# Optimization experiments

Hardware: AMD Instinct MI355X
Metric: run time of the kernel (lower is better)

## Reference

```python
import jax, jax.numpy as jnp
import numpy as np
import math

N, H, E, G = 20000, 256, 320000, 1000
NF, NS = 64, 3           # sinusoid frequencies, spatial dims
DIS = 2 * NF * NS        # 384
EIN = 2 * H + 9 + DIS    # edge MLP input dim = 905


def silu(x):
    return x * jax.nn.sigmoid(x)


def sin_emb(x):
    # x: [E, 3] -> [E, 2*NF*3]
    freqs = 2.0 * math.pi * jnp.arange(NF, dtype=x.dtype)
    emb = (x[..., None] * freqs).reshape(x.shape[0], NF * NS)
    return jnp.concatenate([jnp.sin(emb), jnp.cos(emb)], axis=-1)


def layer_norm(x, gamma, beta, eps=1e-5):
    mu = jnp.mean(x, axis=-1, keepdims=True)
    var = jnp.var(x, axis=-1, keepdims=True)
    return (x - mu) * jax.lax.rsqrt(var + eps) * gamma + beta


def setup_inputs() -> dict:
    key = jax.random.key(0)
    ks = jax.random.split(key, 16)
    s = 0.02
    return {
        "node_features": jax.random.normal(ks[0], (N, H), jnp.float32),
        "lattices": jax.random.normal(ks[1], (G, 3, 3), jnp.float32),
        "edge_index": jax.random.randint(ks[2], (2, E), 0, N, dtype=jnp.int64),
        "edge2graph": jnp.sort(jax.random.randint(ks[3], (E,), 0, G, dtype=jnp.int64)),
        "frac_diff": jax.random.uniform(ks[4], (E, NS), jnp.float32),
        "num_atoms": jax.random.randint(ks[5], (G,), 0, 100, dtype=jnp.int64),
        "ln_gamma": jnp.ones((H,), jnp.float32),
        "ln_beta": jnp.zeros((H,), jnp.float32),
        "We1": jax.random.normal(ks[6], (EIN, H), jnp.float32) * s,
        "be1": jnp.zeros((H,), jnp.float32),
        "We2": jax.random.normal(ks[7], (H, H), jnp.float32) * s,
        "be2": jnp.zeros((H,), jnp.float32),
        "Wn1": jax.random.normal(ks[8], (2 * H, H), jnp.float32) * s,
        "bn1": jnp.zeros((H,), jnp.float32),
        "Wn2": jax.random.normal(ks[9], (H, H), jnp.float32) * s,
        "bn2": jnp.zeros((H,), jnp.float32),
    }


def reference(node_features, lattices, edge_index, edge2graph, frac_diff, num_atoms,
              ln_gamma, ln_beta, We1, be1, We2, be2, Wn1, bn1, Wn2, bn2):
    n = node_features.shape[0]
    h = layer_norm(node_features, ln_gamma, ln_beta)

    # edge model: gather + concat + MLP
    hi = h[edge_index[0]]                      # [E, H]
    hj = h[edge_index[1]]                      # [E, H]
    fd = sin_emb(frac_diff)                    # [E, DIS]
    ltl = jnp.einsum('gij,gkj->gik', lattices, lattices).reshape(-1, 9)  # non_symmetric: L @ L^T
    le = ltl[edge2graph]                       # [E, 9]
    x = jnp.concatenate([hi, hj, le, fd], axis=1)        # [E, EIN]
    e = silu(x @ We1 + be1)
    e = silu(e @ We2 + be2)                    # [E, H]

    # node model: scatter-mean + concat + MLP
    src = edge_index[0]
    sums = jax.ops.segment_sum(e, src, num_segments=n)   # [N, H]
    cnt = jax.ops.segment_sum(jnp.ones((e.shape[0],), e.dtype), src, num_segments=n)
    agg = sums / jnp.maximum(cnt, 1.0)[:, None]
    y = jnp.concatenate([h, agg], axis=1)                # [N, 2H]
    y = silu(y @ Wn1 + bn1)
    y = silu(y @ Wn2 + bn2)

    return node_features + y
```

## Files before the change

kernel.cpp:

```cpp
#include <hip/hip_runtime.h>

typedef unsigned short UST;
typedef __bf16 bf16x8 __attribute__((ext_vector_type(8)));
typedef float floatx4 __attribute__((ext_vector_type(4)));
typedef unsigned short ushort8v __attribute__((ext_vector_type(8)));
typedef unsigned short ushort4v __attribute__((ext_vector_type(4)));

#define N_NODES 20000
#define E_EDGES 320000
#define KE 928
#define M_PAD 20096

static __device__ __forceinline__ UST f2bf(float x){
  unsigned int u = __float_as_uint(x);
  u += 0x7fffu + ((u >> 16) & 1u);
  return (UST)(u >> 16);
}
static __device__ __forceinline__ float bf2f(UST u){
  return __uint_as_float(((unsigned int)u) << 16);
}
static __device__ __forceinline__ float siluf(float v){
  return v / (1.0f + __expf(-v));
}
static __device__ __forceinline__ void gll16(const void* g, void* lds){
  __builtin_amdgcn_global_load_lds(
      (const __attribute__((address_space(1))) unsigned int*)g,
      (__attribute__((address_space(3))) unsigned int*)lds, 16, 0, 0);
}

static __device__ __forceinline__ void mfma_step(const UST* As, const UST* Bs,
    floatx4 (&acc)[4][4], int lm, int quad, int wM, int wN){
  bf16x8 a[4], b[4];
#pragma unroll
  for (int i = 0; i < 4; ++i)
    a[i] = *(const bf16x8*)(As + (wM + i*16 + lm)*32 + quad*8);
#pragma unroll
  for (int i = 0; i < 4; ++i)
    b[i] = *(const bf16x8*)(Bs + (wN + i*16 + lm)*32 + quad*8);
#pragma unroll
  for (int mi = 0; mi < 4; ++mi)
#pragma unroll
    for (int ni = 0; ni < 4; ++ni)
      acc[mi][ni] = __builtin_amdgcn_mfma_f32_16x16x32_bf16(a[mi], b[ni], acc[mi][ni], 0, 0, 0);
}

static __device__ __forceinline__ void mfma_stage2(const UST* At, const UST* Bg,
    int Kb, floatx4 (&acc)[4][4], int lm, int quad, int wM, int wN){
#pragma unroll 2
  for (int k0 = 0; k0 < 256; k0 += 32){
    bf16x8 a[4], b[4];
#pragma unroll
    for (int i = 0; i < 4; ++i)
      a[i] = *(const bf16x8*)(At + (wM + i*16 + lm)*264 + k0 + quad*8);
#pragma unroll
    for (int i = 0; i < 4; ++i)
      b[i] = *(const bf16x8*)(Bg + (size_t)(wN + i*16 + lm)*Kb + k0 + quad*8);
#pragma unroll
    for (int mi = 0; mi < 4; ++mi)
#pragma unroll
      for (int ni = 0; ni < 4; ++ni)
        acc[mi][ni] = __builtin_amdgcn_mfma_f32_16x16x32_bf16(a[mi], b[ni], acc[mi][ni], 0, 0, 0);
  }
}

__global__ __launch_bounds__(256) void prep_all(
    const float* __restrict__ We1, const float* __restrict__ We2,
    const float* __restrict__ Wn1, const float* __restrict__ Wn2,
    const float* __restrict__ x, const float* __restrict__ gamma,
    const float* __restrict__ beta, const float* __restrict__ lat,
    const int* __restrict__ esrc, int* __restrict__ cnti,
    UST* __restrict__ W1T, UST* __restrict__ W2T,
    UST* __restrict__ Wn1T, UST* __restrict__ Wn2T,
    UST* __restrict__ h, float* __restrict__ ltl){
  int bid = blockIdx.x, t = threadIdx.x;
  if (bid < 928){
    int i = bid*256 + t;
    int n = i / KE, k = i % KE;
    float v = 0.0f;
    if (k < 512)      v = We1[(size_t)k*256 + n];
    else if (k < 896){
      int idx = k - 512, j = idx >> 1, b = idx & 1;
      v = We1[(size_t)(521 + b*192 + j)*256 + n];
    }
    else if (k < 905) v = We1[(size_t)(k-384)*256 + n];
    W1T[i] = f2bf(v);
  } else if (bid < 1184){
    int i = (bid-928)*256 + t;
    int n = i >> 8, k = i & 255;
    W2T[i]  = f2bf(We2[(size_t)k*256 + n]);
    Wn2T[i] = f2bf(Wn2[(size_t)k*256 + n]);
  } else if (bid < 1696){
    int i = (bid-1184)*256 + t;
    int n = i >> 9, k = i & 511;
    Wn1T[i] = f2bf(Wn1[(size_t)k*256 + n]);
  } else if (bid < 6696){
    int wave = t >> 6, lane = t & 63;
    int row = (bid-1696)*4 + wave;
    const float4* xp = (const float4*)(x + (size_t)row * 256);
    float4 v = xp[lane];
    float s  = v.x + v.y + v.z + v.w;
    float sq = v.x*v.x + v.y*v.y + v.z*v.z + v.w*v.w;
#pragma unroll
    for (int o = 32; o > 0; o >>= 1){ s += __shfl_xor(s, o); sq += __shfl_xor(sq, o); }
    float mu  = s * (1.0f/256.0f);
    float var = sq * (1.0f/256.0f) - mu*mu;
    float rs  = rsqrtf(var + 1e-5f);
    float4 g = ((const float4*)gamma)[lane];
    float4 b = ((const float4*)beta)[lane];
    ushort4v o4;
    o4[0] = f2bf((v.x-mu)*rs*g.x + b.x);
    o4[1] = f2bf((v.y-mu)*rs*g.y + b.y);
    o4[2] = f2bf((v.z-mu)*rs*g.z + b.z);
    o4[3] = f2bf((v.w-mu)*rs*g.w + b.w);
    *(ushort4v*)(h + (size_t)row*256 + lane*4) = o4;
  } else if (bid < 6732){
    int i = (bid-6696)*256 + t;
    if (i < 9000){
      int g = i / 9, ij = i % 9, a = ij / 3, b = ij % 3;
      const float* L = lat + g*9;
      ltl[i] = L[a*3+0]*L[b*3+0] + L[a*3+1]*L[b*3+1] + L[a*3+2]*L[b*3+2];
    }
  } else {
    int e = (bid-6732)*256 + t;
    if (e < E_EDGES) atomicAdd(&cnti[esrc[e]], 1);
  }
}

__global__ __launch_bounds__(256) void scan_kernel(const int* __restrict__ cnti,
    int* __restrict__ off, int* __restrict__ head){
  __shared__ int ps[256];
  int t = threadIdx.x;
  const int CH = 80;
  const int4* cp = (const int4*)cnti;
  int base = t * CH;
  int s = 0;
#pragma unroll 1
  for (int i = 0; i < CH/4; ++i){
    int4 v = cp[t*(CH/4) + i];
    int idx = base + i*4;
    if (idx   < N_NODES) s += v.x;
    if (idx+1 < N_NODES) s += v.y;
    if (idx+2 < N_NODES) s += v.z;
    if (idx+3 < N_NODES) s += v.w;
  }
  ps[t] = s; __syncthreads();
#pragma unroll 1
  for (int o = 1; o < 256; o <<= 1){
    int v = (t >= o) ? ps[t - o] : 0;
    __syncthreads();
    ps[t] += v;
    __syncthreads();
  }
  int run = (t > 0) ? ps[t-1] : 0;
#pragma unroll 1
  for (int i = 0; i < CH/4; ++i){
    int4 v = cp[t*(CH/4) + i];
    int idx = base + i*4;
    int a4[4] = {v.x, v.y, v.z, v.w};
#pragma unroll
    for (int j = 0; j < 4; ++j){
      int id = idx + j;
      if (id < N_NODES){ off[id] = run; head[id] = run; run += a4[j]; }
    }
  }
  if (t == 255) off[N_NODES] = run;
}

__global__ __launch_bounds__(256) void fill_kernel(const int* __restrict__ src,
    int* __restrict__ head, int* __restrict__ eidx, int* __restrict__ srcs){
  int e = blockIdx.x*256 + threadIdx.x;
  if (e < E_EDGES){
    int s = src[e];
    int p = atomicAdd(&head[s], 1);
    eidx[p] = e;
    srcs[p] = s;
  }
}

__global__ __launch_bounds__(512, 4)
void gemm_edge_fused(const UST* __restrict__ h, const int* __restrict__ ei,
                     const int* __restrict__ e2g, const float* __restrict__ fdif,
                     const float* __restrict__ ltl, const UST* __restrict__ W1T,
                     const float* __restrict__ be1, const int* __restrict__ eidx,
                     const UST* __restrict__ W2T, const float* __restrict__ be2,
                     const int* __restrict__ rownode, float* __restrict__ sums){
  __shared__ __attribute__((aligned(16))) UST lds[128*264];
  __shared__ int rn[128];
  UST* As0 = lds;
  UST* As1 = lds + 4096;
  UST* Bs0 = lds + 8192;
  UST* Bs1 = lds + 16384;
  UST* e1t = lds;
  UST* EsT = lds;
  int t = threadIdx.x;
  int bM = blockIdx.x;
  int rA = t >> 2, cA = (t & 3) * 8;
  int p0 = bM*128 + rA;
  int e0 = eidx[p0];
  int src0 = ei[e0];
  int dst0 = ei[E_EDGES + e0];
  int g0 = e2g[e0];
  float f0x = fdif[e0*3+0], f0y = fdif[e0*3+1], f0z = fdif[e0*3+2];
  size_t btb0 = (size_t)rA*KE + cA;
  size_t btb1 = btb0 + (size_t)128*KE;
  int lane = t & 63, lm = lane & 15, quad = lane >> 4;
  int wave = t >> 6, wM = (wave >> 2)*64, wN = (wave & 3)*64;
  floatx4 acc[4][4] = {};
  UST* a0d = &As0[rA*32 + cA];
  UST* a1d = &As1[rA*32 + cA];
  UST* b0d0 = &Bs0[rA*32 + cA];
  UST* b0d1 = &Bs0[(128+rA)*32 + cA];
  UST* b1d0 = &Bs1[rA*32 + cA];
  UST* b1d1 = &Bs1[(128+rA)*32 + cA];
  if (t < 128) rn[t] = rownode[bM*128 + t];

#pragma unroll 1
  for (int w = 0; w < 8; ++w){
    int k0 = w*64;
    const UST* srow = (w < 4) ? (h + (size_t)src0*256 + k0)
                              : (h + (size_t)dst0*256 + (k0 - 256));
    gll16(srow + cA,      a0d);
    gll16(srow + 32 + cA, a1d);
    gll16(W1T + btb0 + k0,      b0d0);
    gll16(W1T + btb1 + k0,      b0d1);
    gll16(W1T + btb0 + k0 + 32, b1d0);
    gll16(W1T + btb1 + k0 + 32, b1d1);
    __syncthreads();
    mfma_step(As0, Bs0, acc, lm, quad, wM, wN);
    mfma_step(As1, Bs1, acc, lm, quad, wM, wN);
    __syncthreads();
  }
#pragma unroll 1
  for (int w = 8; w < 14; ++w){
    int k0 = w*64;
    gll16(W1T + btb0 + k0,      b0d0);
    gll16(W1T + btb1 + k0,      b0d1);
    gll16(W1T + btb0 + k0 + 32, b1d0);
    gll16(W1T + btb1 + k0 + 32, b1d1);
    int jb0 = (k0 + cA - 512) >> 1;
    ushort8v o0, o1;
#pragma unroll
    for (int ii = 0; ii < 4; ++ii){
      int jj = jb0 + ii;
      int dim = jj >> 6; float kf = (float)(jj & 63);
      float fr = (dim == 0) ? f0x : ((dim == 1) ? f0y : f0z);
      float q = __builtin_amdgcn_fractf(fr * kf);
      o0[2*ii]   = f2bf(__builtin_amdgcn_sinf(q));
      o0[2*ii+1] = f2bf(__builtin_amdgcn_cosf(q));
    }
#pragma unroll
    for (int ii = 0; ii < 4; ++ii){
      int jj = jb0 + 16 + ii;
      int dim = jj >> 6; float kf = (float)(jj & 63);
      float fr = (dim == 0) ? f0x : ((dim == 1) ? f0y : f0z);
      float q = __builtin_amdgcn_fractf(fr * kf);
      o1[2*ii]   = f2bf(__builtin_amdgcn_sinf(q));
      o1[2*ii+1] = f2bf(__builtin_amdgcn_cosf(q));
    }
    *(ushort8v*)a0d = o0;
    *(ushort8v*)a1d = o1;
    __syncthreads();
    mfma_step(As0, Bs0, acc, lm, quad, wM, wN);
    mfma_step(As1, Bs1, acc, lm, quad, wM, wN);
    __syncthreads();
  }
  {
    gll16(W1T + btb0 + 896, b0d0);
    gll16(W1T + btb1 + 896, b0d1);
    ushort8v o0;
#pragma unroll
    for (int i = 0; i < 8; ++i){
      int c = cA + i;
      o0[i] = (c < 9) ? f2bf(ltl[g0*9 + c]) : (UST)0;
    }
    *(ushort8v*)a0d = o0;
    __syncthreads();
    mfma_step(As0, Bs0, acc, lm, quad, wM, wN);
  }
  __syncthreads();
#pragma unroll
  for (int mi = 0; mi < 4; ++mi)
#pragma unroll
    for (int r = 0; r < 4; ++r){
      int ml = wM + mi*16 + quad*4 + r;
#pragma unroll
      for (int ni = 0; ni < 4; ++ni){
        int nl = wN + ni*16 + lm;
        float v = acc[mi][ni][r] + be1[nl];
        e1t[ml*264 + nl] = f2bf(siluf(v));
      }
    }
  __syncthreads();

  floatx4 acc2[4][4] = {};
  mfma_stage2(e1t, W2T, 256, acc2, lm, quad, wM, wN);
  __syncthreads();

#pragma unroll
  for (int mi = 0; mi < 4; ++mi)
#pragma unroll
    for (int ni = 0; ni < 4; ++ni){
      int nl = wN + ni*16 + lm;
      int ml = wM + mi*16 + quad*4;
      ushort4v pk;
#pragma unroll
      for (int r = 0; r < 4; ++r)
        pk[r] = f2bf(siluf(acc2[mi][ni][r] + be2[nl]));
      *(ushort4v*)&EsT[nl*132 + ml] = pk;
    }
  __syncthreads();
  {
    int c = t & 255, hh = t >> 8;
    int rbeg = hh * 64;
    int cur = rn[rbeg];
    float run = 0.0f;
#pragma unroll 1
    for (int r = rbeg; r < rbeg + 64; r += 4){
      ushort4v v4 = *(const ushort4v*)&EsT[c*132 + r];
#pragma unroll
      for (int q2 = 0; q2 < 4; ++q2){
        int nd = rn[r + q2];
        if (nd != cur){ atomicAdd(&sums[(size_t)cur*256 + c], run); run = 0.0f; cur = nd; }
        run += bf2f(v4[q2]);
      }
    }
    atomicAdd(&sums[(size_t)cur*256 + c], run);
  }
}

__global__ __launch_bounds__(512, 4)
void gemm_node12(const UST* __restrict__ h, const float* __restrict__ sums,
                 const int* __restrict__ offs, const UST* __restrict__ B1,
                 const float* __restrict__ bn1, const UST* __restrict__ B2,
                 const float* __restrict__ bn2,
                 float* __restrict__ out_f, const float* __restrict__ resid){
  __shared__ __attribute__((aligned(16))) UST lds[128*264];
  UST* As0 = lds;
  UST* As1 = lds + 4096;
  UST* Bs0 = lds + 8192;
  UST* Bs1 = lds + 16384;
  UST* y1t = lds;
  int t = threadIdx.x;
  int bM = blockIdx.x;
  int rA = t >> 2, cA = (t & 3) * 8;
  int row = bM*128 + rA;
  bool valid = row < N_NODES;
  float inv = 0.0f;
  if (valid){
    int deg = offs[row+1] - offs[row];
    inv = 1.0f / fmaxf((float)deg, 1.0f);
  }
  const UST* hrow = h + (size_t)row*256;
  const float* srow = sums + (size_t)row*256;
  size_t bb0 = (size_t)rA*512 + cA;
  size_t bb1 = bb0 + (size_t)128*512;
  int lane = t & 63, lm = lane & 15, quad = lane >> 4;
  int wave = t >> 6, wM = (wave >> 2)*64, wN = (wave & 3)*64;
  floatx4 acc[4][4] = {};
  UST* a0d = &As0[rA*32 + cA];
  UST* a1d = &As1[rA*32 + cA];
  UST* b0d0 = &Bs0[rA*32 + cA];
  UST* b0d1 = &Bs0[(128+rA)*32 + cA];
  UST* b1d0 = &Bs1[rA*32 + cA];
  UST* b1d1 = &Bs1[(128+rA)*32 + cA];
  const ushort8v z8 = {0,0,0,0,0,0,0,0};
#pragma unroll 1
  for (int w = 0; w < 8; ++w){
    int k0 = w*64;
    if (k0 < 256){
      if (valid){
        gll16(hrow + k0 + cA,      a0d);
        gll16(hrow + k0 + 32 + cA, a1d);
      } else {
        *(ushort8v*)a0d = z8;
        *(ushort8v*)a1d = z8;
      }
    } else {
      ushort8v o0 = z8, o1 = z8;
      if (valid){
        int q = k0 - 256 + cA;
        float4 s0 = *(const float4*)(srow + q);
        float4 s1 = *(const float4*)(srow + q + 4);
        o0[0]=f2bf(s0.x*inv); o0[1]=f2bf(s0.y*inv); o0[2]=f2bf(s0.z*inv); o0[3]=f2bf(s0.w*inv);
        o0[4]=f2bf(s1.x*inv); o0[5]=f2bf(s1.y*inv); o0[6]=f2bf(s1.z*inv); o0[7]=f2bf(s1.w*inv);
        float4 s2 = *(const float4*)(srow + q + 32);
        float4 s3 = *(const float4*)(srow + q + 36);
        o1[0]=f2bf(s2.x*inv); o1[1]=f2bf(s2.y*inv); o1[2]=f2bf(s2.z*inv); o1[3]=f2bf(s2.w*inv);
        o1[4]=f2bf(s3.x*inv); o1[5]=f2bf(s3.y*inv); o1[6]=f2bf(s3.z*inv); o1[7]=f2bf(s3.w*inv);
      }
      *(ushort8v*)a0d = o0;
      *(ushort8v*)a1d = o1;
    }
    gll16(B1 + bb0 + k0,      b0d0);
    gll16(B1 + bb1 + k0,      b0d1);
    gll16(B1 + bb0 + k0 + 32, b1d0);
    gll16(B1 + bb1 + k0 + 32, b1d1);
    __syncthreads();
    mfma_step(As0, Bs0, acc, lm, quad, wM, wN);
    mfma_step(As1, Bs1, acc, lm, quad, wM, wN);
    __syncthreads();
  }
  __syncthreads();
#pragma unroll
  for (int mi = 0; mi < 4; ++mi)
#pragma unroll
    for (int r = 0; r < 4; ++r){
      int ml = wM + mi*16 + quad*4 + r;
#pragma unroll
      for (int ni = 0; ni < 4; ++ni){
        int nl = wN + ni*16 + lm;
        y1t[ml*264 + nl] = f2bf(siluf(acc[mi][ni][r] + bn1[nl]));
      }
    }
  __syncthreads();
  floatx4 acc2[4][4] = {};
  mfma_stage2(y1t, B2, 256, acc2, lm, quad, wM, wN);
  int mbase = bM*128 + wM + quad*4;
  int nbase = wN + lm;
#pragma unroll
  for (int mi = 0; mi < 4; ++mi)
#pragma unroll
    for (int r = 0; r < 4; ++r){
      int m = mbase + mi*16 + r;
      if (m < N_NODES){
#pragma unroll
        for (int ni = 0; ni < 4; ++ni){
          int n = nbase + ni*16;
          float v = siluf(acc2[mi][ni][r] + bn2[n]);
          out_f[(size_t)m*256 + n] = resid[(size_t)m*256 + n] + v;
        }
      }
    }
}

extern "C" void kernel_launch(void* const* d_in, const int* in_sizes, int n_in,
                              void* d_out, int out_size, void* d_ws, size_t ws_size,
                              hipStream_t stream){
  (void)in_sizes; (void)n_in; (void)out_size; (void)ws_size;
  const float* node_features = (const float*)d_in[0];
  const float* lattices      = (const float*)d_in[1];
  const int*   edge_index    = (const int*)d_in[2];
  const int*   edge2graph    = (const int*)d_in[3];
  const float* frac_diff     = (const float*)d_in[4];
  const float* ln_gamma      = (const float*)d_in[6];
  const float* ln_beta       = (const float*)d_in[7];
  const float* We1 = (const float*)d_in[8];
  const float* be1 = (const float*)d_in[9];
  const float* We2 = (const float*)d_in[10];
  const float* be2 = (const float*)d_in[11];
  const float* Wn1 = (const float*)d_in[12];
  const float* bn1 = (const float*)d_in[13];
  const float* Wn2 = (const float*)d_in[14];
  const float* bn2 = (const float*)d_in[15];

  char* w = (char*)d_ws;
  size_t off_b = 0;
  auto carve = [&](size_t bytes) -> char* {
    char* p = w + off_b; off_b += (bytes + 1023) & ~(size_t)1023; return p;
  };
  UST*   W1T  = (UST*)carve((size_t)256*KE*2);
  UST*   W2T  = (UST*)carve((size_t)256*256*2);
  UST*   Wn1T = (UST*)carve((size_t)256*512*2);
  UST*   Wn2T = (UST*)carve((size_t)256*256*2);
  UST*   hbf  = (UST*)carve((size_t)N_NODES*256*2);
  float* ltl  = (float*)carve((size_t)9000*4);
  int*   cnti = (int*)carve((size_t)20480*4);
  int*   offs = (int*)carve((size_t)(N_NODES+1)*4);
  int*   head = (int*)carve((size_t)N_NODES*4);
  int*   eidx = (int*)carve((size_t)E_EDGES*4);
  int*   srcs = (int*)carve((size_t)E_EDGES*4);
  float* sums = (float*)carve((size_t)N_NODES*256*4);

  hipMemsetAsync(cnti, 0, (size_t)20480*4, stream);
  hipMemsetAsync(sums, 0, (size_t)N_NODES*256*4, stream);

  prep_all<<<6732 + E_EDGES/256, 256, 0, stream>>>(We1, We2, Wn1, Wn2,
      node_features, ln_gamma, ln_beta, lattices, edge_index, cnti,
      W1T, W2T, Wn1T, Wn2T, hbf, ltl);

  scan_kernel<<<1, 256, 0, stream>>>(cnti, offs, head);
  fill_kernel<<<E_EDGES/256, 256, 0, stream>>>(edge_index, head, eidx, srcs);

  gemm_edge_fused<<<E_EDGES/128, 512, 0, stream>>>(
      hbf, edge_index, edge2graph, frac_diff, ltl, W1T, be1, eidx,
      W2T, be2, srcs, sums);

  gemm_node12<<<M_PAD/128, 512, 0, stream>>>(
      hbf, sums, offs, Wn1T, bn1, Wn2T, bn2, (float*)d_out, node_features);
}
```

Before: 493.6 us.

## Precompute per-node and per-graph edge-MLP projections to shrink edge GEMM K

Splits the first edge-MLP layer by linearity. The h_src and h_dst parts are computed once per node in a new node-level GEMM (P1 = h @ We1[:512], with N=512 outputs). The lattice and bias parts are folded into a per-graph vector (Pleb). The edge GEMM now only contracts over the 384 sinusoid features and gathers fp32 P1/Pleb rows in its epilogue. This removes the per-edge gather of h and cuts edge GEMM K from 928 to 384. In exchange it adds a ~41MB fp32 P1 buffer and random fp32 gathers in the epilogue, and the hidden inputs now sum in fp32 rather than bf16.

```diff
diff --git a/kernel.cpp b/kernel.cpp
--- a/kernel.cpp
+++ b/kernel.cpp
@@ -8,7 +8,7 @@
 
 #define N_NODES 20000
 #define E_EDGES 320000
-#define KE 928
+#define KF 384
 #define M_PAD 20096
 
 static __device__ __forceinline__ UST f2bf(float x){
@@ -68,34 +68,31 @@
     const float* __restrict__ Wn1, const float* __restrict__ Wn2,
     const float* __restrict__ x, const float* __restrict__ gamma,
     const float* __restrict__ beta, const float* __restrict__ lat,
-    const int* __restrict__ esrc, int* __restrict__ cnti,
+    const int* __restrict__ esrc, const float* __restrict__ be1,
+    int* __restrict__ cnti,
     UST* __restrict__ W1T, UST* __restrict__ W2T,
-    UST* __restrict__ Wn1T, UST* __restrict__ Wn2T,
-    UST* __restrict__ h, float* __restrict__ ltl){
+    UST* __restrict__ Wn1T, UST* __restrict__ Wn2T, UST* __restrict__ W1hT,
+    UST* __restrict__ h, float* __restrict__ Pleb){
   int bid = blockIdx.x, t = threadIdx.x;
-  if (bid < 928){
+  if (bid < 384){
     int i = bid*256 + t;
-    int n = i / KE, k = i % KE;
-    float v = 0.0f;
-    if (k < 512)      v = We1[(size_t)k*256 + n];
-    else if (k < 896){
-      int idx = k - 512, j = idx >> 1, b = idx & 1;
-      v = We1[(size_t)(521 + b*192 + j)*256 + n];
-    }
-    else if (k < 905) v = We1[(size_t)(k-384)*256 + n];
-    W1T[i] = f2bf(v);
-  } else if (bid < 1184){
-    int i = (bid-928)*256 + t;
+    int n = i / KF, k = i % KF;
+    W1T[i] = f2bf(We1[(size_t)(521 + (k&1)*192 + (k>>1))*256 + n]);
+  } else if (bid < 640){
+    int i = (bid-384)*256 + t;
     int n = i >> 8, k = i & 255;
     W2T[i]  = f2bf(We2[(size_t)k*256 + n]);
     Wn2T[i] = f2bf(Wn2[(size_t)k*256 + n]);
-  } else if (bid < 1696){
-    int i = (bid-1184)*256 + t;
+  } else if (bid < 1152){
+    int i = (bid-640)*256 + t;
     int n = i >> 9, k = i & 511;
     Wn1T[i] = f2bf(Wn1[(size_t)k*256 + n]);
-  } else if (bid < 6696){
+  } else if (bid < 1664){
+    int n = bid - 1152, k = t;
+    W1hT[n*256 + k] = f2bf(We1[(size_t)(k + (n & 256))*256 + (n & 255)]);
+  } else if (bid < 6664){
     int wave = t >> 6, lane = t & 63;
-    int row = (bid-1696)*4 + wave;
+    int row = (bid-1664)*4 + wave;
     const float4* xp = (const float4*)(x + (size_t)row * 256);
     float4 v = xp[lane];
     float s  = v.x + v.y + v.z + v.w;
@@ -113,15 +110,20 @@
     o4[2] = f2bf((v.z-mu)*rs*g.z + b.z);
     o4[3] = f2bf((v.w-mu)*rs*g.w + b.w);
     *(ushort4v*)(h + (size_t)row*256 + lane*4) = o4;
-  } else if (bid < 6732){
-    int i = (bid-6696)*256 + t;
-    if (i < 9000){
-      int g = i / 9, ij = i % 9, a = ij / 3, b = ij % 3;
-      const float* L = lat + g*9;
-      ltl[i] = L[a*3+0]*L[b*3+0] + L[a*3+1]*L[b*3+1] + L[a*3+2]*L[b*3+2];
-    }
+  } else if (bid < 7664){
+    int g = bid - 6664;
+    const float* L = lat + g*9;
+    float acc = be1[t];
+#pragma unroll
+    for (int a = 0; a < 3; ++a)
+#pragma unroll
+      for (int b = 0; b < 3; ++b){
+        float ltlv = L[a*3+0]*L[b*3+0] + L[a*3+1]*L[b*3+1] + L[a*3+2]*L[b*3+2];
+        acc += ltlv * We1[(size_t)(512 + a*3 + b)*256 + t];
+      }
+    Pleb[g*256 + t] = acc;
   } else {
-    int e = (bid-6732)*256 + t;
+    int e = (bid-7664)*256 + t;
     if (e < E_EDGES) atomicAdd(&cnti[esrc[e]], 1);
   }
 }
@@ -178,14 +180,66 @@
 }
 
 __global__ __launch_bounds__(512, 4)
-void gemm_edge_fused(const UST* __restrict__ h, const int* __restrict__ ei,
-                     const int* __restrict__ e2g, const float* __restrict__ fdif,
-                     const float* __restrict__ ltl, const UST* __restrict__ W1T,
-                     const float* __restrict__ be1, const int* __restrict__ eidx,
+void gemm_p1(const UST* __restrict__ h, const UST* __restrict__ B1,
+             float* __restrict__ P1){
+  __shared__ __attribute__((aligned(16))) UST lds[24576];
+  UST* As0 = lds;
+  UST* As1 = lds + 4096;
+  UST* Bs0 = lds + 8192;
+  UST* Bs1 = lds + 16384;
+  int t = threadIdx.x;
+  int bM = blockIdx.x >> 1, bN = (blockIdx.x & 1) << 8;
+  int rA = t >> 2, cA = (t & 3) * 8;
+  const UST* hrow = h + (size_t)(bM*128 + rA)*256;
+  size_t bb0 = (size_t)(bN + rA)*256 + cA;
+  size_t bb1 = bb0 + (size_t)128*256;
+  int lane = t & 63, lm = lane & 15, quad = lane >> 4;
+  int wave = t >> 6, wM = (wave >> 2)*64, wN = (wave & 3)*64;
+  floatx4 acc[4][4] = {};
+  UST* a0d = &As0[rA*32 + cA];
+  UST* a1d = &As1[rA*32 + cA];
+  UST* b0d0 = &Bs0[rA*32 + cA];
+  UST* b0d1 = &Bs0[(128+rA)*32 + cA];
+  UST* b1d0 = &Bs1[rA*32 + cA];
+  UST* b1d1 = &Bs1[(128+rA)*32 + cA];
+#pragma unroll 1
+  for (int w = 0; w < 4; ++w){
+    int k0 = w*64;
+    gll16(hrow + k0 + cA,      a0d);
+    gll16(hrow + k0 + 32 + cA, a1d);
+    gll16(B1 + bb0 + k0,      b0d0);
+    gll16(B1 + bb1 + k0,      b0d1);
+    gll16(B1 + bb0 + k0 + 32, b1d0);
+    gll16(B1 + bb1 + k0 + 32, b1d1);
+    __syncthreads();
+    mfma_step(As0, Bs0, acc, lm, quad, wM, wN);
+    mfma_step(As1, Bs1, acc, lm, quad, wM, wN);
+    __syncthreads();
+  }
+  int mbase = bM*128 + wM + quad*4;
+#pragma unroll
+  for (int mi = 0; mi < 4; ++mi)
+#pragma unroll
+    for (int r = 0; r < 4; ++r){
+      int m = mbase + mi*16 + r;
+#pragma unroll
+      for (int ni = 0; ni < 4; ++ni){
+        int n = bN + wN + ni*16 + lm;
+        P1[(size_t)m*512 + n] = acc[mi][ni][r];
+      }
+    }
+}
+
+__global__ __launch_bounds__(512, 4)
+void gemm_edge_fused(const int* __restrict__ ei, const int* __restrict__ e2g,
+                     const float* __restrict__ fdif, const UST* __restrict__ W1T,
+                     const int* __restrict__ eidx,
                      const UST* __restrict__ W2T, const float* __restrict__ be2,
-                     const int* __restrict__ rownode, float* __restrict__ sums){
+                     const int* __restrict__ rownode,
+                     const float* __restrict__ P1, const float* __restrict__ Pleb,
+                     float* __restrict__ sums){
   __shared__ __attribute__((aligned(16))) UST lds[128*264];
-  __shared__ int rn[128];
+  __shared__ int rn[128], rd[128], rg[128];
   UST* As0 = lds;
   UST* As1 = lds + 4096;
   UST* Bs0 = lds + 8192;
@@ -197,12 +251,9 @@
   int rA = t >> 2, cA = (t & 3) * 8;
   int p0 = bM*128 + rA;
   int e0 = eidx[p0];
-  int src0 = ei[e0];
-  int dst0 = ei[E_EDGES + e0];
-  int g0 = e2g[e0];
   float f0x = fdif[e0*3+0], f0y = fdif[e0*3+1], f0z = fdif[e0*3+2];
-  size_t btb0 = (size_t)rA*KE + cA;
-  size_t btb1 = btb0 + (size_t)128*KE;
+  size_t btb0 = (size_t)rA*KF + cA;
+  size_t btb1 = btb0 + (size_t)128*KF;
   int lane = t & 63, lm = lane & 15, quad = lane >> 4;
   int wave = t >> 6, wM = (wave >> 2)*64, wN = (wave & 3)*64;
   floatx4 acc[4][4] = {};
@@ -212,32 +263,21 @@
   UST* b0d1 = &Bs0[(128+rA)*32 + cA];
   UST* b1d0 = &Bs1[rA*32 + cA];
   UST* b1d1 = &Bs1[(128+rA)*32 + cA];
-  if (t < 128) rn[t] = rownode[bM*128 + t];
-
-#pragma unroll 1
-  for (int w = 0; w < 8; ++w){
-    int k0 = w*64;
-    const UST* srow = (w < 4) ? (h + (size_t)src0*256 + k0)
-                              : (h + (size_t)dst0*256 + (k0 - 256));
-    gll16(srow + cA,      a0d);
-    gll16(srow + 32 + cA, a1d);
-    gll16(W1T + btb0 + k0,      b0d0);
-    gll16(W1T + btb1 + k0,      b0d1);
-    gll16(W1T + btb0 + k0 + 32, b1d0);
-    gll16(W1T + btb1 + k0 + 32, b1d1);
-    __syncthreads();
-    mfma_step(As0, Bs0, acc, lm, quad, wM, wN);
-    mfma_step(As1, Bs1, acc, lm, quad, wM, wN);
-    __syncthreads();
-  }
-#pragma unroll 1
-  for (int w = 8; w < 14; ++w){
+  if (t < 128){
+    int e = eidx[bM*128 + t];
+    rn[t] = rownode[bM*128 + t];
+    rd[t] = ei[E_EDGES + e];
+    rg[t] = e2g[e];
+  }
+
+#pragma unroll 1
+  for (int w = 0; w < 6; ++w){
     int k0 = w*64;
     gll16(W1T + btb0 + k0,      b0d0);
     gll16(W1T + btb1 + k0,      b0d1);
     gll16(W1T + btb0 + k0 + 32, b1d0);
     gll16(W1T + btb1 + k0 + 32, b1d1);
-    int jb0 = (k0 + cA - 512) >> 1;
+    int jb0 = (k0 + cA) >> 1;
     ushort8v o0, o1;
 #pragma unroll
     for (int ii = 0; ii < 4; ++ii){
@@ -264,29 +304,20 @@
     mfma_step(As1, Bs1, acc, lm, quad, wM, wN);
     __syncthreads();
   }
-  {
-    gll16(W1T + btb0 + 896, b0d0);
-    gll16(W1T + btb1 + 896, b0d1);
-    ushort8v o0;
-#pragma unroll
-    for (int i = 0; i < 8; ++i){
-      int c = cA + i;
-      o0[i] = (c < 9) ? f2bf(ltl[g0*9 + c]) : (UST)0;
-    }
-    *(ushort8v*)a0d = o0;
-    __syncthreads();
-    mfma_step(As0, Bs0, acc, lm, quad, wM, wN);
-  }
-  __syncthreads();
+
 #pragma unroll
   for (int mi = 0; mi < 4; ++mi)
 #pragma unroll
     for (int r = 0; r < 4; ++r){
       int ml = wM + mi*16 + quad*4 + r;
+      int s = rn[ml], d = rd[ml], g = rg[ml];
+      const float* ps = P1 + (size_t)s*512;
+      const float* pd = P1 + (size_t)d*512 + 256;
+      const float* pg = Pleb + (size_t)g*256;
 #pragma unroll
       for (int ni = 0; ni < 4; ++ni){
         int nl = wN + ni*16 + lm;
-        float v = acc[mi][ni][r] + be1[nl];
+        float v = acc[mi][ni][r] + ps[nl] + pd[nl] + pg[nl];
         e1t[ml*264 + nl] = f2bf(siluf(v));
       }
     }
@@ -458,12 +489,14 @@
   auto carve = [&](size_t bytes) -> char* {
     char* p = w + off_b; off_b += (bytes + 1023) & ~(size_t)1023; return p;
   };
-  UST*   W1T  = (UST*)carve((size_t)256*KE*2);
+  UST*   W1T  = (UST*)carve((size_t)256*KF*2);
   UST*   W2T  = (UST*)carve((size_t)256*256*2);
   UST*   Wn1T = (UST*)carve((size_t)256*512*2);
   UST*   Wn2T = (UST*)carve((size_t)256*256*2);
-  UST*   hbf  = (UST*)carve((size_t)N_NODES*256*2);
-  float* ltl  = (float*)carve((size_t)9000*4);
+  UST*   W1hT = (UST*)carve((size_t)512*256*2);
+  UST*   hbf  = (UST*)carve((size_t)M_PAD*256*2);
+  float* P1   = (float*)carve((size_t)M_PAD*512*4);
+  float* Pleb = (float*)carve((size_t)1000*256*4);
   int*   cnti = (int*)carve((size_t)20480*4);
   int*   offs = (int*)carve((size_t)(N_NODES+1)*4);
   int*   head = (int*)carve((size_t)N_NODES*4);
@@ -474,16 +507,17 @@
   hipMemsetAsync(cnti, 0, (size_t)20480*4, stream);
   hipMemsetAsync(sums, 0, (size_t)N_NODES*256*4, stream);
 
-  prep_all<<<6732 + E_EDGES/256, 256, 0, stream>>>(We1, We2, Wn1, Wn2,
-      node_features, ln_gamma, ln_beta, lattices, edge_index, cnti,
-      W1T, W2T, Wn1T, Wn2T, hbf, ltl);
+  prep_all<<<7664 + E_EDGES/256, 256, 0, stream>>>(We1, We2, Wn1, Wn2,
+      node_features, ln_gamma, ln_beta, lattices, edge_index, be1, cnti,
+      W1T, W2T, Wn1T, Wn2T, W1hT, hbf, Pleb);
 
   scan_kernel<<<1, 256, 0, stream>>>(cnti, offs, head);
   fill_kernel<<<E_EDGES/256, 256, 0, stream>>>(edge_index, head, eidx, srcs);
 
+  gemm_p1<<<(M_PAD/128)*2, 512, 0, stream>>>(hbf, W1hT, P1);
+
   gemm_edge_fused<<<E_EDGES/128, 512, 0, stream>>>(
-      hbf, edge_index, edge2graph, frac_diff, ltl, W1T, be1, eidx,
-      W2T, be2, srcs, sums);
+      edge_index, edge2graph, frac_diff, W1T, eidx, W2T, be2, srcs, P1, Pleb, sums);
 
   gemm_node12<<<M_PAD/128, 512, 0, stream>>>(
       hbf, sums, offs, Wn1T, bn1, Wn2T, bn2, (float*)d_out, node_features);
```

Result: faster. 449.6 us (-8.9%).
